# Kernel tuning notes

Hardware: AMD Instinct MI355X
Metric: run time of the kernel (lower is better)

Reference implementation:

```python
import jax, jax.numpy as jnp
import numpy as np

WIN, SHIFT = 8, 4
DIM, HEADS, MLP_H = 96, 6, 384
B, H, W = 1, 512, 512
HEAD_D = DIM // HEADS
N = WIN * WIN
EPS = 1e-5


def _rel_pos_index():
    ch = np.arange(WIN)
    coords = np.stack(np.meshgrid(ch, ch, indexing='ij')).reshape(2, -1)  # [2, 64]
    rel = (coords[:, :, None] - coords[:, None, :]).transpose(1, 2, 0)    # [64, 64, 2]
    rel[:, :, 0] += WIN - 1
    rel[:, :, 1] += WIN - 1
    rel[:, :, 0] *= 2 * WIN - 1
    return rel.sum(-1)


def _attn_mask():
    img = np.zeros((H, W))
    cnt = 0
    for hs in (slice(0, -WIN), slice(-WIN, -SHIFT), slice(-SHIFT, None)):
        for ws in (slice(0, -WIN), slice(-WIN, -SHIFT), slice(-SHIFT, None)):
            img[hs, ws] = cnt
            cnt += 1
    mw = img.reshape(H // WIN, WIN, W // WIN, WIN).transpose(0, 2, 1, 3).reshape(-1, N)
    diff = mw[:, None, :] - mw[:, :, None]
    return np.where(diff != 0, -100.0, 0.0).astype(np.float32)  # [nW, 64, 64]


REL_IDX = jnp.asarray(_rel_pos_index())
ATTN_MASK = jnp.asarray(_attn_mask())


def layernorm(x, w, b):
    mu = jnp.mean(x, axis=-1, keepdims=True)
    var = jnp.mean(jnp.square(x - mu), axis=-1, keepdims=True)
    return (x - mu) * jax.lax.rsqrt(var + EPS) * w + b


def setup_inputs() -> dict:
    key = jax.random.key(0)
    ks = jax.random.split(key, 16)
    s = 0.02
    return {
        'x': jax.random.normal(ks[0], (B, DIM, H, W), jnp.float32),
        'norm1_w': jnp.ones((DIM,), jnp.float32),
        'norm1_b': jnp.zeros((DIM,), jnp.float32),
        'qkv_w': jax.random.normal(ks[1], (3 * DIM, DIM), jnp.float32) * s,
        'qkv_b': jnp.zeros((3 * DIM,), jnp.float32),
        'rpb': jax.random.normal(ks[2], ((2 * WIN - 1) ** 2, HEADS), jnp.float32) * s,
        'proj_w': jax.random.normal(ks[3], (DIM, DIM), jnp.float32) * s,
        'proj_b': jnp.zeros((DIM,), jnp.float32),
        'norm2_w': jnp.ones((DIM,), jnp.float32),
        'norm2_b': jnp.zeros((DIM,), jnp.float32),
        'fc1_w': jax.random.normal(ks[4], (MLP_H, DIM), jnp.float32) * s,
        'fc1_b': jnp.zeros((MLP_H,), jnp.float32),
        'fc2_w': jax.random.normal(ks[5], (DIM, MLP_H), jnp.float32) * s,
        'fc2_b': jnp.zeros((DIM,), jnp.float32),
    }


def reference(x, norm1_w, norm1_b, qkv_w, qkv_b, rpb, proj_w, proj_b,
              norm2_w, norm2_b, fc1_w, fc1_b, fc2_w, fc2_b):
    nH, nW_ = H // WIN, W // WIN
    nWin = nH * nW_
    shortcut = jnp.transpose(x, (0, 2, 3, 1))            # [B,H,W,C]
    xn = layernorm(shortcut, norm1_w, norm1_b)
    xs = jnp.roll(xn, (-SHIFT, -SHIFT), axis=(1, 2))     # cyclic shift
    # window partition -> [B*nWin, N, C]
    win = xs.reshape(B, nH, WIN, nW_, WIN, DIM).transpose(0, 1, 3, 2, 4, 5)
    win = win.reshape(B * nWin, N, DIM)
    qkv = win @ qkv_w.T + qkv_b                          # [Bw, N, 3C]
    qkv = qkv.reshape(-1, N, 3, HEADS, HEAD_D).transpose(2, 0, 3, 1, 4)
    q, k, v = qkv[0], qkv[1], qkv[2]                     # [Bw, h, N, d]
    scale = HEAD_D ** -0.5
    attn = jnp.einsum('bhnd,bhmd->bhnm', q * scale, k)   # [Bw, h, 64, 64]
    bias = rpb[REL_IDX.reshape(-1)].reshape(N, N, HEADS).transpose(2, 0, 1)
    attn = attn + bias[None]
    attn = attn.reshape(B, nWin, HEADS, N, N) + ATTN_MASK[None, :, None]
    attn = jax.nn.softmax(attn.reshape(-1, HEADS, N, N), axis=-1)
    out = jnp.einsum('bhnm,bhmd->bhnd', attn, v).transpose(0, 2, 1, 3).reshape(-1, N, DIM)
    out = out @ proj_w.T + proj_b
    # window reverse + un-shift
    out = out.reshape(B, nH, nW_, WIN, WIN, DIM).transpose(0, 1, 3, 2, 4, 5).reshape(B, H, W, DIM)
    out = jnp.roll(out, (SHIFT, SHIFT), axis=(1, 2))
    x1 = shortcut + out
    h = layernorm(x1, norm2_w, norm2_b)
    h = jax.nn.gelu(h @ fc1_w.T + fc1_b, approximate=False) @ fc2_w.T + fc2_b
    x2 = x1 + h
    return jnp.transpose(x2, (0, 3, 1, 2))               # [B,C,H,W]
```

## Files before the change

kernel.cpp:

```cpp
#include <hip/hip_runtime.h>
#include <math.h>

#define WINSZ  8
#define SHIFTV 4
#define DIM    96
#define HEADS  6
#define HEAD_D 16
#define MLP_H  384
#define HH     512
#define WWID   512
#define HWSZ   (HH*WWID)
#define NTOK   64
#define EPSV   1e-5f
#define XP     97
#define QP     17
#define BFP    120

#define L2E    1.44269504088896f
#define QSC    0.360673760222f

#define OFF_W1   0
#define OFF_W2   36864
#define OFF_QKV  73728
#define OFF_PROJ 101376
#define OFF_BIAS 110592
#define WS_FULL  208896
#define WS_MLP   73728

#define QKP 104
#define VTP 72
#define X1P 97
#define WBP 104

#define WBA_OFF 13312
#define WBB_OFF 23296
#define SMEM_SZ 40448

typedef __attribute__((ext_vector_type(2))) short  s2v;
typedef __attribute__((ext_vector_type(4))) short  s4v;
typedef __attribute__((ext_vector_type(8))) short  s8v;
typedef __attribute__((ext_vector_type(4))) float  f4v;
typedef __attribute__((ext_vector_type(4))) unsigned short u4v;

__device__ __forceinline__ unsigned short f2bf(float v) {
    union { float f; unsigned u; } c; c.f = v;
    unsigned r = c.u + 0x7fffu + ((c.u >> 16) & 1u);
    return (unsigned short)(r >> 16);
}
__device__ __forceinline__ float bf2f(unsigned short u) {
    union { unsigned u; float f; } c; c.u = ((unsigned)u) << 16; return c.f;
}
__device__ __forceinline__ unsigned pk2(float a, float b) {
    unsigned r;
    asm("v_cvt_pk_bf16_f32 %0, %1, %2" : "=v"(r) : "v"(a), "v"(b));
    return r;
}
__device__ __forceinline__ s4v pk4(f4v v) {
    union { unsigned u[2]; s4v s; } o;
    o.u[0] = pk2(v[0], v[1]);
    o.u[1] = pk2(v[2], v[3]);
    return o.s;
}
__device__ __forceinline__ float fexp2(float x) {
#if __has_builtin(__builtin_amdgcn_exp2f)
    return __builtin_amdgcn_exp2f(x);
#else
    return exp2f(x);
#endif
}
__device__ __forceinline__ unsigned long long shfl64(unsigned long long v, int src) {
    union { unsigned long long q; int i[2]; } c; c.q = v;
    c.i[0] = __shfl(c.i[0], src);
    c.i[1] = __shfl(c.i[1], src);
    return c.q;
}
__device__ __forceinline__ float fast_gelu(float h) {
    float h2 = h*h;
    float u  = fmaf(0.044715f, h2, 1.0f);
    float e  = fexp2(-2.3022082f * h * u);
    return h * __builtin_amdgcn_rcpf(1.0f + e);
}

__device__ __forceinline__ void gld_lds16(const void* g, void* l) {
    __builtin_amdgcn_global_load_lds(
        (const __attribute__((address_space(1))) unsigned*)(g),
        (__attribute__((address_space(3))) unsigned*)(l),
        16, 0, 0);
}

__device__ __forceinline__ void stage48(const char* gb, int stride_b,
                                        char* wb, int tid) {
    #pragma unroll
    for (int k = 0; k < 3; ++k) {
        int idx = tid + k*256;
        if (k < 2 || idx < 624) {
            int r   = idx / 13;
            int rem = idx - r*13;
            const char* src = (rem < 12) ? (gb + r*stride_b + rem*16) : gb;
            char* dst = wb + ((tid & ~63) + k*256)*16;
            gld_lds16(src, dst);
        }
    }
}

__device__ __forceinline__ void stage_chunk(const char* w1B, const char* w2B,
                                            int n, char* dst, int tid) {
    int ch = n >> 2, s = n & 3;
    const char* src; int stride;
    if      (s == 0) { src = w1B + ch*96*192;            stride = 192; }
    else if (s == 1) { src = w1B + ch*96*192 + 48*192;   stride = 192; }
    else if (s == 2) { src = w2B + ch*192;               stride = 768; }
    else             { src = w2B + ch*192 + 48*768;      stride = 768; }
    stage48(src, stride, dst, tid);
}

__global__ __launch_bounds__(256) void conv_all(
    const float* __restrict__ qkvw, const float* __restrict__ projw,
    const float* __restrict__ f1w,  const float* __restrict__ f2w,
    const float* __restrict__ rpb,  short* __restrict__ ws)
{
    int i = (blockIdx.x*256 + threadIdx.x)*4;
    if (i < 110592) {
        const float* src; int off;
        if (i < 36864)       { src = f1w;  off = i;          }
        else if (i < 73728)  { src = f2w;  off = i - 36864;  }
        else if (i < 101376) { src = qkvw; off = i - 73728;  }
        else                 { src = projw; off = i - 101376; }
        f4v v = *(const f4v*)&src[off];
        s4v o;
        #pragma unroll
        for (int j = 0; j < 4; ++j) o[j] = (short)f2bf(v[j]);
        *(s4v*)&ws[i] = o;
    } else if (i < WS_FULL) {
        int idx = i - 110592;
        int tb = idx / 24576;
        int rm = idx - tb*24576;
        int hd = rm >> 12;
        int rc = rm & 4095;
        int r = rc >> 6, c0 = rc & 63;
        int rti = r>>3, rtj = r&7;
        int bh = tb>>1, bw = tb&1;
        int rhr = bh ? (rti<4?1:2) : 0;
        int rwr = bw ? (rtj<4?1:2) : 0;
        s4v o;
        #pragma unroll
        for (int j = 0; j < 4; ++j) {
            int c = c0 + j;
            int cti = c>>3, ctj = c&7;
            int rel = (rti-cti+7)*15 + (rtj-ctj+7);
            float b = rpb[rel*HEADS + hd];
            int rhc = bh ? (cti<4?1:2) : 0;
            int rwc = bw ? (ctj<4?1:2) : 0;
            if (rhr != rhc || rwr != rwc) b -= 100.f;
            o[j] = (short)f2bf(b * L2E);
        }
        *(s4v*)&ws[OFF_BIAS + idx] = o;
    }
}

__global__ __launch_bounds__(256,4) void fused_kernel(
    const float* __restrict__ x,
    const float* __restrict__ n1w, const float* __restrict__ n1b,
    const float* __restrict__ qkvb, const float* __restrict__ projb,
    const float* __restrict__ n2w, const float* __restrict__ n2b,
    const float* __restrict__ f1b, const float* __restrict__ f2b,
    const short* __restrict__ wqkv, const short* __restrict__ wproj,
    const short* __restrict__ w1b, const short* __restrict__ w2b,
    const short* __restrict__ btab,
    float* __restrict__ out)
{
    __shared__ __align__(16) char smem[SMEM_SZ];
    short* qb   = (short*)smem;
    short* kb2  = (short*)(smem + 13312);
    short* vT   = (short*)(smem + 26624);
    short* aob  = qb;
    short* lnb2 = (short*)smem;
    short* hid  = (short*)smem;
    short* wbA  = (short*)(smem + WBA_OFF);
    short* wbB  = (short*)(smem + WBB_OFF);
    float* x1f  = (float*)smem;

    const int tid  = threadIdx.x;
    const int wv   = tid >> 6, lane = tid & 63;
    const int col  = lane & 15, kq = lane >> 4;
    const int trow = wv*16 + col;

    int bid = blockIdx.x;
    int wl = (bid & 7)*512 + ((bid >> 5) << 2) + ((bid >> 3) & 3);
    const int wi = wl >> 6, wj = wl & 63;

    const int ti = trow>>3, tj = trow&7;
    const int hpos = (wi*8 + ti + SHIFTV) & (HH-1);
    const int wpos = (wj*8 + tj + SHIFTV) & (WWID-1);
    const int p = hpos*WWID + wpos;

    s8v bfr[3];
    {
        float v[24], s1 = 0.f, s2 = 0.f;
        #pragma unroll
        for (int kb = 0; kb < 3; ++kb)
            #pragma unroll
            for (int j = 0; j < 8; ++j) {
                float vv = x[(kb*32 + kq*8 + j)*HWSZ + p];
                v[kb*8+j] = vv; s1 += vv; s2 += vv*vv;
            }
        s1 += __shfl_xor(s1, 16); s2 += __shfl_xor(s2, 16);
        s1 += __shfl_xor(s1, 32); s2 += __shfl_xor(s2, 32);
        float mu = s1*(1.f/96.f);
        float rs = rsqrtf(s2*(1.f/96.f) - mu*mu + EPSV);
        #pragma unroll
        for (int kb = 0; kb < 3; ++kb) {
            f4v wA = *(const f4v*)&n1w[kb*32 + kq*8];
            f4v wB = *(const f4v*)&n1w[kb*32 + kq*8 + 4];
            f4v bA = *(const f4v*)&n1b[kb*32 + kq*8];
            f4v bB = *(const f4v*)&n1b[kb*32 + kq*8 + 4];
            float a[8];
            #pragma unroll
            for (int j = 0; j < 4; ++j) {
                a[j]   = (v[kb*8+j]  -mu)*rs*wA[j] + bA[j];
                a[4+j] = (v[kb*8+4+j]-mu)*rs*wB[j] + bB[j];
            }
            union { unsigned u[4]; s8v s; } o;
            #pragma unroll
            for (int j = 0; j < 4; ++j) o.u[j] = pk2(a[2*j], a[2*j+1]);
            bfr[kb] = o.s;
        }
    }

    float shc[24];
    #pragma unroll
    for (int mt = 0; mt < 6; ++mt)
        #pragma unroll
        for (int i = 0; i < 4; ++i)
            shc[mt*4+i] = x[(mt*16 + kq*4 + i)*HWSZ + p];

    const s8v zfrag = {0,0,0,0,0,0,0,0};

    {
        #pragma unroll
        for (int g = 0; g < 6; ++g) {
            s8v aw[9];
            #pragma unroll
            for (int m = 0; m < 3; ++m)
                #pragma unroll
                for (int kb = 0; kb < 3; ++kb)
                    aw[m*3+kb] = *(const s8v*)&wqkv[((g*3+m)*16+col)*96 + kb*32 + kq*8];
            #pragma unroll
            for (int m = 0; m < 3; ++m) {
                int mt = g*3 + m;
                f4v acc = {0.f,0.f,0.f,0.f};
                #pragma unroll
                for (int kb = 0; kb < 3; ++kb)
                    acc = __builtin_amdgcn_mfma_f32_16x16x32_bf16(aw[m*3+kb], bfr[kb], acc, 0,0,0);
                int od0 = mt*16 + kq*4;
                f4v bia = *(const f4v*)&qkvb[od0];
                if (mt < 6) {
                    f4v t;
                    #pragma unroll
                    for (int i = 0; i < 4; ++i) t[i] = (acc[i]+bia[i])*QSC;
                    *(s4v*)&qb[trow*QKP + od0] = pk4(t);
                } else if (mt < 12) {
                    f4v t;
                    #pragma unroll
                    for (int i = 0; i < 4; ++i) t[i] = acc[i]+bia[i];
                    *(s4v*)&kb2[trow*QKP + od0 - 96] = pk4(t);
                } else {
                    int d0 = od0 - 192;
                    f4v t;
                    #pragma unroll
                    for (int i = 0; i < 4; ++i) t[i] = acc[i]+bia[i];
                    s4v o = pk4(t);
                    #pragma unroll
                    for (int i = 0; i < 4; ++i)
                        vT[(d0+i)*VTP + trow] = o[i];
                }
            }
        }
    }
    __syncthreads();

    const int tb = ((wi==63)?2:0) | ((wj==63)?1:0);
    u4v bt[4];
    {
        const short* gb = btab + ((tb*6+0)<<12) + (trow<<6);
        #pragma unroll
        for (int mt = 0; mt < 4; ++mt) bt[mt] = *(const u4v*)&gb[mt*16 + kq*4];
    }
    for (int hd = 0; hd < 6; ++hd) {
        u4v btn[4];
        if (hd < 5) {
            const short* gb = btab + ((tb*6+hd+1)<<12) + (trow<<6);
            #pragma unroll
            for (int mt = 0; mt < 4; ++mt) btn[mt] = *(const u4v*)&gb[mt*16 + kq*4];
        }
        s8v bq = zfrag;
        if (kq < 2) bq = *(const s8v*)&qb[trow*QKP + hd*16 + kq*8];
        f4v st[4];
        #pragma unroll
        for (int mt = 0; mt < 4; ++mt) {
            s8v a = zfrag;
            if (kq < 2) a = *(const s8v*)&kb2[(mt*16+col)*QKP + hd*16 + kq*8];
            f4v z = {0.f,0.f,0.f,0.f};
            st[mt] = __builtin_amdgcn_mfma_f32_16x16x32_bf16(a, bq, z, 0,0,0);
        }
        float pe[16];
        #pragma unroll
        for (int mt = 0; mt < 4; ++mt)
            #pragma unroll
            for (int i = 0; i < 4; ++i)
                pe[mt*4+i] = fexp2(st[mt][i] + bf2f(bt[mt][i]));
        float s8r[8];
        #pragma unroll
        for (int j = 0; j < 8; ++j) s8r[j] = pe[2*j] + pe[2*j+1];
        #pragma unroll
        for (int j = 0; j < 4; ++j) s8r[j] += s8r[j+4];
        float sum = (s8r[0]+s8r[2]) + (s8r[1]+s8r[3]);
        sum += __shfl_xor(sum, 16);
        sum += __shfl_xor(sum, 32);
        unsigned long long p64[4];
        #pragma unroll
        for (int mt = 0; mt < 4; ++mt) {
            union { unsigned u[2]; unsigned long long q; } pq;
            pq.u[0] = pk2(pe[mt*4+0], pe[mt*4+1]);
            pq.u[1] = pk2(pe[mt*4+2], pe[mt*4+3]);
            p64[mt] = pq.q;
        }
        const int s0 = col + ((kq & 1) << 5);
        const int sel = kq >> 1;
        f4v g = {0.f,0.f,0.f,0.f};
        #pragma unroll
        for (int c = 0; c < 2; ++c) {
            unsigned long long t0 = shfl64(p64[2*c],   s0);
            unsigned long long t1 = shfl64(p64[2*c+1], s0);
            unsigned long long lo = sel ? t1 : t0;
            unsigned long long u0 = shfl64(p64[2*c],   s0+16);
            unsigned long long u1 = shfl64(p64[2*c+1], s0+16);
            unsigned long long hi = sel ? u1 : u0;
            union { unsigned long long q[2]; s8v v; } bb;
            bb.q[0] = lo; bb.q[1] = hi;
            s8v a = *(const s8v*)&vT[(hd*16+col)*VTP + c*32 + kq*8];
            g = __builtin_amdgcn_mfma_f32_16x16x32_bf16(a, bb.v, g, 0,0,0);
        }
        float linv = __builtin_amdgcn_rcpf(sum);
        f4v gl;
        #pragma unroll
        for (int i = 0; i < 4; ++i) gl[i] = g[i]*linv;
        *(s4v*)&aob[trow*QKP + hd*16 + kq*4] = pk4(gl);
        #pragma unroll
        for (int mt = 0; mt < 4; ++mt) bt[mt] = btn[mt];
    }
    __syncthreads();

    stage_chunk((const char*)w1b, (const char*)w2b, 0, (char*)wbA, tid);
    stage_chunk((const char*)w1b, (const char*)w2b, 1, (char*)wbB, tid);

    float x1r[24];
    {
        s8v bfr2[3];
        #pragma unroll
        for (int kb = 0; kb < 3; ++kb)
            bfr2[kb] = *(const s8v*)&aob[trow*QKP + kb*32 + kq*8];
        #pragma unroll
        for (int g = 0; g < 2; ++g) {
            s8v aw[9];
            #pragma unroll
            for (int m = 0; m < 3; ++m)
                #pragma unroll
                for (int kb = 0; kb < 3; ++kb)
                    aw[m*3+kb] = *(const s8v*)&wproj[((g*3+m)*16+col)*96 + kb*32 + kq*8];
            #pragma unroll
            for (int m = 0; m < 3; ++m) {
                int mt = g*3 + m;
                f4v acc = {0.f,0.f,0.f,0.f};
                #pragma unroll
                for (int kb = 0; kb < 3; ++kb)
                    acc = __builtin_amdgcn_mfma_f32_16x16x32_bf16(aw[m*3+kb], bfr2[kb], acc, 0,0,0);
                int c0 = mt*16 + kq*4;
                f4v pb4 = *(const f4v*)&projb[c0];
                #pragma unroll
                for (int i = 0; i < 4; ++i)
                    x1r[mt*4+i] = shc[mt*4+i] + acc[i] + pb4[i];
            }
        }
    }

    const int mrow = wv*16;

    {
        float s1 = 0.f, s2 = 0.f;
        #pragma unroll
        for (int j = 0; j < 24; ++j) { s1 += x1r[j]; s2 += x1r[j]*x1r[j]; }
        s1 += __shfl_xor(s1, 16); s2 += __shfl_xor(s2, 16);
        s1 += __shfl_xor(s1, 32); s2 += __shfl_xor(s2, 32);
        float mu = s1*(1.f/96.f);
        float rs = rsqrtf(s2*(1.f/96.f) - mu*mu + EPSV);
        #pragma unroll
        for (int mt = 0; mt < 6; ++mt) {
            int c0 = mt*16 + kq*4;
            f4v w4 = *(const f4v*)&n2w[c0];
            f4v b4 = *(const f4v*)&n2b[c0];
            f4v t;
            #pragma unroll
            for (int i = 0; i < 4; ++i)
                t[i] = (x1r[mt*4+i]-mu)*rs*w4[i] + b4[i];
            *(s4v*)&lnb2[trow*QKP + c0] = pk4(t);
        }
    }
    __threadfence_block();

    s8v a1[3];
    #pragma unroll
    for (int kb = 0; kb < 3; ++kb)
        a1[kb] = *(const s8v*)&lnb2[(mrow+col)*QKP + kb*32 + kq*8];

    f4v acc2[6];
    #pragma unroll
    for (int n = 0; n < 6; ++n) acc2[n] = (f4v){0.f,0.f,0.f,0.f};

    __syncthreads();

    #pragma unroll
    for (int ch = 0; ch < 4; ++ch) {
        #pragma unroll
        for (int sub = 0; sub < 2; ++sub) {
            const int cidx = ch*4 + sub;
            const short* wb = (cidx & 1) ? wbB : wbA;
            #pragma unroll
            for (int nl = 0; nl < 3; ++nl) {
                f4v acc = (f4v){0.f,0.f,0.f,0.f};
                #pragma unroll
                for (int kb = 0; kb < 3; ++kb) {
                    s8v b = *(const s8v*)&wb[(nl*16+col)*WBP + kb*32 + kq*8];
                    acc = __builtin_amdgcn_mfma_f32_16x16x32_bf16(a1[kb], b, acc, 0,0,0);
                }
                int cch = sub*48 + nl*16 + col;
                float bias = f1b[ch*96 + cch];
                f4v t;
                #pragma unroll
                for (int i = 0; i < 4; ++i) t[i] = fast_gelu(acc[i]+bias);
                s4v o = pk4(t);
                #pragma unroll
                for (int i = 0; i < 4; ++i)
                    hid[(mrow + kq*4 + i)*QKP + cch] = o[i];
            }
            __syncthreads();
            if (cidx + 2 < 16)
                stage_chunk((const char*)w1b, (const char*)w2b, cidx+2,
                            (char*)((cidx & 1) ? wbB : wbA), tid);
        }
        s8v a2[3];
        #pragma unroll
        for (int kb = 0; kb < 3; ++kb)
            a2[kb] = *(const s8v*)&hid[(mrow+col)*QKP + kb*32 + kq*8];
        #pragma unroll
        for (int sub = 0; sub < 2; ++sub) {
            const int cidx = ch*4 + 2 + sub;
            const short* wb = (cidx & 1) ? wbB : wbA;
            #pragma unroll
            for (int nl = 0; nl < 3; ++nl) {
                int nt = sub*3 + nl;
                #pragma unroll
                for (int kb = 0; kb < 3; ++kb) {
                    s8v b = *(const s8v*)&wb[(nl*16+col)*WBP + kb*32 + kq*8];
                    acc2[nt] = __builtin_amdgcn_mfma_f32_16x16x32_bf16(a2[kb], b, acc2[nt], 0,0,0);
                }
            }
            __syncthreads();
            if (cidx + 2 < 16)
                stage_chunk((const char*)w1b, (const char*)w2b, cidx+2,
                            (char*)((cidx & 1) ? wbB : wbA), tid);
        }
    }

    #pragma unroll
    for (int mt = 0; mt < 6; ++mt) {
        #pragma unroll
        for (int i = 0; i < 4; ++i)
            x1f[trow*X1P + mt*16 + kq*4 + i] = x1r[mt*4+i];
    }
    __threadfence_block();
    #pragma unroll
    for (int nt = 0; nt < 6; ++nt) {
        int c = nt*16 + col;
        float bias = f2b[c];
        #pragma unroll
        for (int i = 0; i < 4; ++i) {
            int t = mrow + kq*4 + i;
            x1f[t*X1P + c] += acc2[nt][i] + bias;
        }
    }
    __threadfence_block();
    {
        int tt = mrow + col;
        int tti = tt>>3, ttj = tt&7;
        int pp = ((wi*8 + tti + SHIFTV) & (HH-1))*WWID + ((wj*8 + ttj + SHIFTV) & (WWID-1));
        #pragma unroll
        for (int it = 0; it < 24; ++it) {
            int c = it*4 + kq;
            out[c*HWSZ + pp] = x1f[tt*X1P + c];
        }
    }
}

__global__ __launch_bounds__(256) void attn_kernel(
    const float* __restrict__ x,
    const float* __restrict__ n1w, const float* __restrict__ n1b,
    const float* __restrict__ qkvw, const float* __restrict__ qkvb,
    const float* __restrict__ rpb,
    const float* __restrict__ projw, const float* __restrict__ projb,
    float* __restrict__ out)
{
    __shared__ float xn[NTOK*XP];
    __shared__ float ao[NTOK*XP];
    __shared__ float qh[NTOK*QP];
    __shared__ float kh[NTOK*QP];
    __shared__ float vh[NTOK*QP];
    __shared__ int   srid[NTOK];
    __shared__ int   spos[NTOK];

    const int tid = threadIdx.x;
    const int blk = blockIdx.x;
    const int wi = blk >> 6, wj = blk & 63;

    {
        int t  = tid >> 2;
        int j4 = tid & 3;
        int ti = t >> 3, tj = t & 7;
        int a = wi*WINSZ + ti;
        int bcol = wj*WINSZ + tj;
        int h = (a + SHIFTV) & (HH-1);
        int w = (bcol + SHIFTV) & (WWID-1);
        int p = h*WWID + w;
        if (j4 == 0) {
            spos[t] = p;
            int rh = (a < HH-WINSZ) ? 0 : (a < HH-SHIFTV ? 1 : 2);
            int rw = (bcol < WWID-WINSZ) ? 0 : (bcol < WWID-SHIFTV ? 1 : 2);
            srid[t] = rh*3 + rw;
        }
        float xv[24];
        float s1 = 0.f, s2 = 0.f;
        int c0 = j4*24;
        #pragma unroll
        for (int i = 0; i < 24; ++i) {
            float v = x[(c0+i)*HWSZ + p];
            xv[i] = v; s1 += v; s2 += v*v;
        }
        s1 += __shfl_xor(s1,1); s2 += __shfl_xor(s2,1);
        s1 += __shfl_xor(s1,2); s2 += __shfl_xor(s2,2);
        float mu  = s1 * (1.f/96.f);
        float var = s2 * (1.f/96.f) - mu*mu;
        float rs  = rsqrtf(var + EPSV);
        #pragma unroll
        for (int i = 0; i < 24; ++i) {
            int c = c0 + i;
            xn[t*XP + c] = (xv[i]-mu)*rs*n1w[c] + n1b[c];
        }
    }
    __syncthreads();

    const int wv   = tid >> 6;
    const int lane = tid & 63;
    const int r    = tid >> 2;
    const int g    = tid & 3;
    const int rti  = r >> 3, rtj = r & 7;

    for (int hd = 0; hd < HEADS; ++hd) {
        for (int it = 0; it < 12; ++it) {
            int ol = it*4 + wv;
            int s = ol >> 4, d = ol & 15;
            int grow = __builtin_amdgcn_readfirstlane(s*DIM + hd*HEAD_D + d);
            const float* wr = qkvw + grow*DIM;
            float acc = qkvb[grow];
            #pragma unroll 8
            for (int c = 0; c < DIM; ++c)
                acc = fmaf(xn[lane*XP+c], wr[c], acc);
            float* dst = (s==0) ? qh : ((s==1) ? kh : vh);
            dst[lane*QP + d] = acc;
        }
        __syncthreads();

        float qr[16];
        #pragma unroll
        for (int d = 0; d < 16; ++d) qr[d] = qh[r*QP+d];
        float scr[16];
        int myrid = srid[r];
        #pragma unroll
        for (int jj = 0; jj < 16; ++jj) {
            int colx = g*16 + jj;
            float a = 0.f;
            #pragma unroll
            for (int d = 0; d < 16; ++d) a = fmaf(qr[d], kh[colx*QP+d], a);
            int cti = colx >> 3, ctj = colx & 7;
            int rel = (rti - cti + 7)*15 + (rtj - ctj + 7);
            float b = rpb[rel*HEADS + hd];
            float m = (srid[colx]==myrid) ? 0.f : -100.f;
            scr[jj] = a*0.25f + b + m;
        }
        float mx = scr[0];
        #pragma unroll
        for (int jj = 1; jj < 16; ++jj) mx = fmaxf(mx, scr[jj]);
        mx = fmaxf(mx, __shfl_xor(mx,1));
        mx = fmaxf(mx, __shfl_xor(mx,2));
        float sum = 0.f;
        #pragma unroll
        for (int jj = 0; jj < 16; ++jj) { scr[jj] = __expf(scr[jj]-mx); sum += scr[jj]; }
        sum += __shfl_xor(sum,1);
        sum += __shfl_xor(sum,2);
        float inv = 1.f/sum;
        #pragma unroll
        for (int d = 0; d < 16; ++d) {
            float a = 0.f;
            #pragma unroll
            for (int jj = 0; jj < 16; ++jj) a = fmaf(scr[jj], vh[(g*16+jj)*QP+d], a);
            a += __shfl_xor(a,1);
            a += __shfl_xor(a,2);
            if (g == 0) ao[r*XP + hd*HEAD_D + d] = a*inv;
        }
        __syncthreads();
    }

    for (int it = 0; it < 24; ++it) {
        int c = __builtin_amdgcn_readfirstlane(it*4 + wv);
        const float* wr = projw + c*DIM;
        float acc = projb[c];
        #pragma unroll 8
        for (int k = 0; k < DIM; ++k)
            acc = fmaf(ao[lane*XP+k], wr[k], acc);
        int p2 = spos[lane];
        float shc = x[c*HWSZ + p2];
        out[c*HWSZ + p2] = shc + acc;
    }
}

__global__ __launch_bounds__(256) void mlp_mfma(
    float* __restrict__ io,
    const float* __restrict__ n2w, const float* __restrict__ n2b,
    const short* __restrict__ w1b, const float* __restrict__ f1b,
    const short* __restrict__ w2b, const float* __restrict__ f2b)
{
    __shared__ short lnbuf[64*BFP];
    __shared__ __align__(16) char ubuf[64*XP*4];
    float* lnf = (float*)ubuf;
    short* hbc = (short*)ubuf;

    const int tid  = threadIdx.x;
    const int base = blockIdx.x * 64;

    for (int idx = tid; idx < 64*DIM; idx += 256) {
        int c = idx >> 6, t = idx & 63;
        lnf[t*XP + c] = io[c*HWSZ + base + t];
    }
    __syncthreads();
    {
        int t = tid >> 2, q = tid & 3;
        float xv[24], s1 = 0.f, s2 = 0.f;
        #pragma unroll
        for (int i = 0; i < 24; ++i) {
            float v = lnf[t*XP + q*24 + i]; xv[i] = v; s1 += v; s2 += v*v;
        }
        s1 += __shfl_xor(s1,1); s2 += __shfl_xor(s2,1);
        s1 += __shfl_xor(s1,2); s2 += __shfl_xor(s2,2);
        float mu = s1*(1.f/96.f);
        float rs = rsqrtf(s2*(1.f/96.f) - mu*mu + EPSV);
        #pragma unroll
        for (int i = 0; i < 24; ++i) {
            int c = q*24 + i;
            lnbuf[t*BFP + c] = (short)f2bf((xv[i]-mu)*rs*n2w[c] + n2b[c]);
        }
    }
    __syncthreads();

    const int l = tid & 63, wv = tid >> 6;
    const int mrow = wv*16;
    const int col = l & 15, kq = l >> 4;

    s8v a1[3];
    #pragma unroll
    for (int kb = 0; kb < 3; ++kb)
        a1[kb] = *(const s8v*)&lnbuf[(mrow+col)*BFP + kb*32 + kq*8];

    f4v acc2[6];
    #pragma unroll
    for (int n = 0; n < 6; ++n) acc2[n] = (f4v){0.f,0.f,0.f,0.f};

    for (int ch = 0; ch < 4; ++ch) {
        #pragma unroll
        for (int nt = 0; nt < 6; ++nt) {
            int n0 = ch*96 + nt*16;
            f4v acc = (f4v){0.f,0.f,0.f,0.f};
            #pragma unroll
            for (int kb = 0; kb < 3; ++kb) {
                s8v b = *(const s8v*)&w1b[(n0+col)*96 + kb*32 + kq*8];
                acc = __builtin_amdgcn_mfma_f32_16x16x32_bf16(a1[kb], b, acc, 0, 0, 0);
            }
            float bias = f1b[n0+col];
            #pragma unroll
            for (int i = 0; i < 4; ++i) {
                float g = fast_gelu(acc[i] + bias);
                hbc[(mrow + kq*4 + i)*BFP + nt*16 + col] = (short)f2bf(g);
            }
        }
        __threadfence_block();
        s8v a2[3];
        #pragma unroll
        for (int kb = 0; kb < 3; ++kb)
            a2[kb] = *(const s8v*)&hbc[(mrow+col)*BFP + kb*32 + kq*8];
        #pragma unroll
        for (int nt = 0; nt < 6; ++nt) {
            #pragma unroll
            for (int kb = 0; kb < 3; ++kb) {
                s8v b = *(const s8v*)&w2b[(nt*16+col)*MLP_H + ch*96 + kb*32 + kq*8];
                acc2[nt] = __builtin_amdgcn_mfma_f32_16x16x32_bf16(a2[kb], b, acc2[nt], 0, 0, 0);
            }
        }
        __threadfence_block();
    }

    #pragma unroll
    for (int nt = 0; nt < 6; ++nt) {
        int c = nt*16 + col;
        float bias = f2b[c];
        #pragma unroll
        for (int i = 0; i < 4; ++i) {
            int t = mrow + kq*4 + i;
            float* p = &io[c*HWSZ + base + t];
            *p = *p + acc2[nt][i] + bias;
        }
    }
}

__global__ __launch_bounds__(256) void conv_w(
    const float* __restrict__ f1w, const float* __restrict__ f2w,
    short* __restrict__ ws)
{
    int i = blockIdx.x*256 + threadIdx.x;
    if (i < 36864)      ws[i] = (short)f2bf(f1w[i]);
    else if (i < 73728) ws[i] = (short)f2bf(f2w[i-36864]);
}

extern "C" void kernel_launch(void* const* d_in, const int* in_sizes, int n_in,
                              void* d_out, int out_size, void* d_ws, size_t ws_size,
                              hipStream_t stream) {
    const float* x     = (const float*)d_in[0];
    const float* n1w   = (const float*)d_in[1];
    const float* n1b   = (const float*)d_in[2];
    const float* qkvw  = (const float*)d_in[3];
    const float* qkvb  = (const float*)d_in[4];
    const float* rpb   = (const float*)d_in[5];
    const float* projw = (const float*)d_in[6];
    const float* projb = (const float*)d_in[7];
    const float* n2w   = (const float*)d_in[8];
    const float* n2b   = (const float*)d_in[9];
    const float* f1w   = (const float*)d_in[10];
    const float* f1b   = (const float*)d_in[11];
    const float* f2w   = (const float*)d_in[12];
    const float* f2b   = (const float*)d_in[13];
    float* out = (float*)d_out;

    if (ws_size >= (size_t)WS_FULL * sizeof(short)) {
        short* wsb = (short*)d_ws;
        hipLaunchKernelGGL(conv_all, dim3(204), dim3(256), 0, stream,
                           qkvw, projw, f1w, f2w, rpb, wsb);
        hipLaunchKernelGGL(fused_kernel, dim3(4096), dim3(256), 0, stream,
                           x, n1w, n1b, qkvb, projb, n2w, n2b, f1b, f2b,
                           wsb + OFF_QKV, wsb + OFF_PROJ,
                           wsb + OFF_W1, wsb + OFF_W2, wsb + OFF_BIAS, out);
    } else {
        short* wsb = (short*)d_ws;
        hipLaunchKernelGGL(attn_kernel, dim3(4096), dim3(256), 0, stream,
                           x, n1w, n1b, qkvw, qkvb, rpb, projw, projb, out);
        hipLaunchKernelGGL(conv_w, dim3(288), dim3(256), 0, stream, f1w, f2w, wsb);
        hipLaunchKernelGGL(mlp_mfma, dim3(4096), dim3(256), 0, stream,
                           out, n2w, n2b, wsb, f1b, wsb + 36864, f2b);
    }
}
```

Measured before the change: 391.9 us.

## Load MLP weights directly to registers with double-buffered prefetch instead of LDS staging

```diff
diff --git a/kernel.cpp b/kernel.cpp
--- a/kernel.cpp
+++ b/kernel.cpp
@@ -29,11 +29,8 @@
 
 #define QKP 104
 #define VTP 72
-#define X1P 97
-#define WBP 104
-
-#define WBA_OFF 13312
-#define WBB_OFF 23296
+#define X1P 100
+
 #define SMEM_SZ 40448
 
 typedef __attribute__((ext_vector_type(2))) short  s2v;
@@ -79,39 +76,6 @@
     float u  = fmaf(0.044715f, h2, 1.0f);
     float e  = fexp2(-2.3022082f * h * u);
     return h * __builtin_amdgcn_rcpf(1.0f + e);
-}
-
-__device__ __forceinline__ void gld_lds16(const void* g, void* l) {
-    __builtin_amdgcn_global_load_lds(
-        (const __attribute__((address_space(1))) unsigned*)(g),
-        (__attribute__((address_space(3))) unsigned*)(l),
-        16, 0, 0);
-}
-
-__device__ __forceinline__ void stage48(const char* gb, int stride_b,
-                                        char* wb, int tid) {
-    #pragma unroll
-    for (int k = 0; k < 3; ++k) {
-        int idx = tid + k*256;
-        if (k < 2 || idx < 624) {
-            int r   = idx / 13;
-            int rem = idx - r*13;
-            const char* src = (rem < 12) ? (gb + r*stride_b + rem*16) : gb;
-            char* dst = wb + ((tid & ~63) + k*256)*16;
-            gld_lds16(src, dst);
-        }
-    }
-}
-
-__device__ __forceinline__ void stage_chunk(const char* w1B, const char* w2B,
-                                            int n, char* dst, int tid) {
-    int ch = n >> 2, s = n & 3;
-    const char* src; int stride;
-    if      (s == 0) { src = w1B + ch*96*192;            stride = 192; }
-    else if (s == 1) { src = w1B + ch*96*192 + 48*192;   stride = 192; }
-    else if (s == 2) { src = w2B + ch*192;               stride = 768; }
-    else             { src = w2B + ch*192 + 48*768;      stride = 768; }
-    stage48(src, stride, dst, tid);
 }
 
 __global__ __launch_bounds__(256) void conv_all(
@@ -174,16 +138,15 @@
     short* kb2  = (short*)(smem + 13312);
     short* vT   = (short*)(smem + 26624);
     short* aob  = qb;
-    short* lnb2 = (short*)smem;
-    short* hid  = (short*)smem;
-    short* wbA  = (short*)(smem + WBA_OFF);
-    short* wbB  = (short*)(smem + WBB_OFF);
-    float* x1f  = (float*)smem;
+    short* lnb2 = qb;
+    short* hid  = qb;
+    float* x1p  = (float*)(smem + 13312);
 
     const int tid  = threadIdx.x;
     const int wv   = tid >> 6, lane = tid & 63;
     const int col  = lane & 15, kq = lane >> 4;
     const int trow = wv*16 + col;
+    const int mrow = wv*16;
 
     int bid = blockIdx.x;
     int wl = (bid & 7)*512 + ((bid >> 5) << 2) + ((bid >> 3) & 3);
@@ -237,21 +200,21 @@
     const s8v zfrag = {0,0,0,0,0,0,0,0};
 
     {
-        #pragma unroll
-        for (int g = 0; g < 6; ++g) {
-            s8v aw[9];
+        auto qkv_pre = [&](int g, s8v (&w)[9]) {
             #pragma unroll
             for (int m = 0; m < 3; ++m)
                 #pragma unroll
                 for (int kb = 0; kb < 3; ++kb)
-                    aw[m*3+kb] = *(const s8v*)&wqkv[((g*3+m)*16+col)*96 + kb*32 + kq*8];
+                    w[m*3+kb] = *(const s8v*)&wqkv[((g*3+m)*16+col)*96 + kb*32 + kq*8];
+        };
+        auto qkv_cmp = [&](int g, const s8v (&w)[9]) {
             #pragma unroll
             for (int m = 0; m < 3; ++m) {
                 int mt = g*3 + m;
                 f4v acc = {0.f,0.f,0.f,0.f};
                 #pragma unroll
                 for (int kb = 0; kb < 3; ++kb)
-                    acc = __builtin_amdgcn_mfma_f32_16x16x32_bf16(aw[m*3+kb], bfr[kb], acc, 0,0,0);
+                    acc = __builtin_amdgcn_mfma_f32_16x16x32_bf16(w[m*3+kb], bfr[kb], acc, 0,0,0);
                 int od0 = mt*16 + kq*4;
                 f4v bia = *(const f4v*)&qkvb[od0];
                 if (mt < 6) {
@@ -275,6 +238,15 @@
                         vT[(d0+i)*VTP + trow] = o[i];
                 }
             }
+        };
+        s8v qwA[9], qwB[9];
+        qkv_pre(0, qwA);
+        #pragma unroll
+        for (int gp = 0; gp < 3; ++gp) {
+            qkv_pre(2*gp+1, qwB);
+            qkv_cmp(2*gp,   qwA);
+            if (gp < 2) qkv_pre(2*gp+2, qwA);
+            qkv_cmp(2*gp+1, qwB);
         }
     }
     __syncthreads();
@@ -351,40 +323,31 @@
     }
     __syncthreads();
 
-    stage_chunk((const char*)w1b, (const char*)w2b, 0, (char*)wbA, tid);
-    stage_chunk((const char*)w1b, (const char*)w2b, 1, (char*)wbB, tid);
-
     float x1r[24];
     {
         s8v bfr2[3];
         #pragma unroll
         for (int kb = 0; kb < 3; ++kb)
             bfr2[kb] = *(const s8v*)&aob[trow*QKP + kb*32 + kq*8];
-        #pragma unroll
-        for (int g = 0; g < 2; ++g) {
-            s8v aw[9];
-            #pragma unroll
-            for (int m = 0; m < 3; ++m)
-                #pragma unroll
-                for (int kb = 0; kb < 3; ++kb)
-                    aw[m*3+kb] = *(const s8v*)&wproj[((g*3+m)*16+col)*96 + kb*32 + kq*8];
-            #pragma unroll
-            for (int m = 0; m < 3; ++m) {
-                int mt = g*3 + m;
-                f4v acc = {0.f,0.f,0.f,0.f};
-                #pragma unroll
-                for (int kb = 0; kb < 3; ++kb)
-                    acc = __builtin_amdgcn_mfma_f32_16x16x32_bf16(aw[m*3+kb], bfr2[kb], acc, 0,0,0);
-                int c0 = mt*16 + kq*4;
-                f4v pb4 = *(const f4v*)&projb[c0];
-                #pragma unroll
-                for (int i = 0; i < 4; ++i)
-                    x1r[mt*4+i] = shc[mt*4+i] + acc[i] + pb4[i];
-            }
-        }
-    }
-
-    const int mrow = wv*16;
+        s8v pw[18];
+        #pragma unroll
+        for (int mt = 0; mt < 6; ++mt)
+            #pragma unroll
+            for (int kb = 0; kb < 3; ++kb)
+                pw[mt*3+kb] = *(const s8v*)&wproj[(mt*16+col)*96 + kb*32 + kq*8];
+        #pragma unroll
+        for (int mt = 0; mt < 6; ++mt) {
+            f4v acc = {0.f,0.f,0.f,0.f};
+            #pragma unroll
+            for (int kb = 0; kb < 3; ++kb)
+                acc = __builtin_amdgcn_mfma_f32_16x16x32_bf16(pw[mt*3+kb], bfr2[kb], acc, 0,0,0);
+            int c0 = mt*16 + kq*4;
+            f4v pb4 = *(const f4v*)&projb[c0];
+            #pragma unroll
+            for (int i = 0; i < 4; ++i)
+                x1r[mt*4+i] = shc[mt*4+i] + acc[i] + pb4[i];
+        }
+    }
 
     {
         float s1 = 0.f, s2 = 0.f;
@@ -408,32 +371,46 @@
     }
     __threadfence_block();
 
-    s8v a1[3];
+    #pragma unroll
+    for (int mt = 0; mt < 6; ++mt) {
+        f4v t;
+        #pragma unroll
+        for (int i = 0; i < 4; ++i) t[i] = x1r[mt*4+i];
+        *(f4v*)&x1p[trow*X1P + mt*16 + kq*4] = t;
+    }
+
+    s8v a1[3], a2[3];
     #pragma unroll
     for (int kb = 0; kb < 3; ++kb)
         a1[kb] = *(const s8v*)&lnb2[(mrow+col)*QKP + kb*32 + kq*8];
+    __threadfence_block();
 
     f4v acc2[6];
     #pragma unroll
     for (int n = 0; n < 6; ++n) acc2[n] = (f4v){0.f,0.f,0.f,0.f};
 
-    __syncthreads();
-
-    #pragma unroll
-    for (int ch = 0; ch < 4; ++ch) {
-        #pragma unroll
-        for (int sub = 0; sub < 2; ++sub) {
-            const int cidx = ch*4 + sub;
-            const short* wb = (cidx & 1) ? wbB : wbA;
+    auto mlp_pre = [&](int ph, s8v (&w)[9]) {
+        const int ch = ph >> 2, q = ph & 3;
+        #pragma unroll
+        for (int nl = 0; nl < 3; ++nl)
+            #pragma unroll
+            for (int kb = 0; kb < 3; ++kb) {
+                if (q < 2)
+                    w[nl*3+kb] = *(const s8v*)&w1b[(ch*96 + q*48 + nl*16 + col)*96 + kb*32 + kq*8];
+                else
+                    w[nl*3+kb] = *(const s8v*)&w2b[((q-2)*48 + nl*16 + col)*MLP_H + ch*96 + kb*32 + kq*8];
+            }
+    };
+    auto mlp_phase = [&](int ph, const s8v (&w)[9]) {
+        const int ch = ph >> 2, q = ph & 3;
+        if (q < 2) {
             #pragma unroll
             for (int nl = 0; nl < 3; ++nl) {
                 f4v acc = (f4v){0.f,0.f,0.f,0.f};
                 #pragma unroll
-                for (int kb = 0; kb < 3; ++kb) {
-                    s8v b = *(const s8v*)&wb[(nl*16+col)*WBP + kb*32 + kq*8];
-                    acc = __builtin_amdgcn_mfma_f32_16x16x32_bf16(a1[kb], b, acc, 0,0,0);
-                }
-                int cch = sub*48 + nl*16 + col;
+                for (int kb = 0; kb < 3; ++kb)
+                    acc = __builtin_amdgcn_mfma_f32_16x16x32_bf16(a1[kb], w[nl*3+kb], acc, 0,0,0);
+                int cch = q*48 + nl*16 + col;
                 float bias = f1b[ch*96 + cch];
                 f4v t;
                 #pragma unroll
@@ -443,41 +420,35 @@
                 for (int i = 0; i < 4; ++i)
                     hid[(mrow + kq*4 + i)*QKP + cch] = o[i];
             }
-            __syncthreads();
-            if (cidx + 2 < 16)
-                stage_chunk((const char*)w1b, (const char*)w2b, cidx+2,
-                            (char*)((cidx & 1) ? wbB : wbA), tid);
-        }
-        s8v a2[3];
-        #pragma unroll
-        for (int kb = 0; kb < 3; ++kb)
-            a2[kb] = *(const s8v*)&hid[(mrow+col)*QKP + kb*32 + kq*8];
-        #pragma unroll
-        for (int sub = 0; sub < 2; ++sub) {
-            const int cidx = ch*4 + 2 + sub;
-            const short* wb = (cidx & 1) ? wbB : wbA;
+            if (q == 1) {
+                __threadfence_block();
+                #pragma unroll
+                for (int kb = 0; kb < 3; ++kb)
+                    a2[kb] = *(const s8v*)&hid[(mrow+col)*QKP + kb*32 + kq*8];
+            }
+        } else {
             #pragma unroll
             for (int nl = 0; nl < 3; ++nl) {
-                int nt = sub*3 + nl;
+                int nt = (q-2)*3 + nl;
                 #pragma unroll
-                for (int kb = 0; kb < 3; ++kb) {
-                    s8v b = *(const s8v*)&wb[(nl*16+col)*WBP + kb*32 + kq*8];
-                    acc2[nt] = __builtin_amdgcn_mfma_f32_16x16x32_bf16(a2[kb], b, acc2[nt], 0,0,0);
-                }
-            }
-            __syncthreads();
-            if (cidx + 2 < 16)
-                stage_chunk((const char*)w1b, (const char*)w2b, cidx+2,
-                            (char*)((cidx & 1) ? wbB : wbA), tid);
-        }
-    }
-
-    #pragma unroll
-    for (int mt = 0; mt < 6; ++mt) {
-        #pragma unroll
-        for (int i = 0; i < 4; ++i)
-            x1f[trow*X1P + mt*16 + kq*4 + i] = x1r[mt*4+i];
-    }
+                for (int kb = 0; kb < 3; ++kb)
+                    acc2[nt] = __builtin_amdgcn_mfma_f32_16x16x32_bf16(a2[kb], w[nl*3+kb], acc2[nt], 0,0,0);
+            }
+        }
+    };
+
+    {
+        s8v wA[9], wB[9];
+        mlp_pre(0, wA);
+        #pragma unroll
+        for (int pp = 0; pp < 8; ++pp) {
+            mlp_pre(2*pp+1, wB);
+            mlp_phase(2*pp, wA);
+            if (pp < 7) mlp_pre(2*pp+2, wA);
+            mlp_phase(2*pp+1, wB);
+        }
+    }
+
     __threadfence_block();
     #pragma unroll
     for (int nt = 0; nt < 6; ++nt) {
@@ -486,7 +457,7 @@
         #pragma unroll
         for (int i = 0; i < 4; ++i) {
             int t = mrow + kq*4 + i;
-            x1f[t*X1P + c] += acc2[nt][i] + bias;
+            x1p[t*X1P + c] += acc2[nt][i] + bias;
         }
     }
     __threadfence_block();
@@ -497,7 +468,7 @@
         #pragma unroll
         for (int it = 0; it < 24; ++it) {
             int c = it*4 + kq;
-            out[c*HWSZ + pp] = x1f[tt*X1P + c];
+            out[c*HWSZ + pp] = x1p[tt*X1P + c];
         }
     }
 }
```

Result: slower. 544.6 us (+39.0%).

## Stage full 96-row MLP weight chunks, halving barriers in the MLP loop

Applied to the files above, without the earlier changes.

```diff
diff --git a/kernel.cpp b/kernel.cpp
--- a/kernel.cpp
+++ b/kernel.cpp
@@ -33,8 +33,8 @@
 #define WBP 104
 
 #define WBA_OFF 13312
-#define WBB_OFF 23296
-#define SMEM_SZ 40448
+#define WBB_OFF 33280
+#define SMEM_SZ 53248
 
 typedef __attribute__((ext_vector_type(2))) short  s2v;
 typedef __attribute__((ext_vector_type(4))) short  s4v;
@@ -88,12 +88,12 @@
         16, 0, 0);
 }
 
-__device__ __forceinline__ void stage48(const char* gb, int stride_b,
+__device__ __forceinline__ void stage96(const char* gb, int stride_b,
                                         char* wb, int tid) {
     #pragma unroll
-    for (int k = 0; k < 3; ++k) {
+    for (int k = 0; k < 5; ++k) {
         int idx = tid + k*256;
-        if (k < 2 || idx < 624) {
+        if (k < 4 || idx < 1248) {
             int r   = idx / 13;
             int rem = idx - r*13;
             const char* src = (rem < 12) ? (gb + r*stride_b + rem*16) : gb;
@@ -103,15 +103,11 @@
     }
 }
 
-__device__ __forceinline__ void stage_chunk(const char* w1B, const char* w2B,
-                                            int n, char* dst, int tid) {
-    int ch = n >> 2, s = n & 3;
-    const char* src; int stride;
-    if      (s == 0) { src = w1B + ch*96*192;            stride = 192; }
-    else if (s == 1) { src = w1B + ch*96*192 + 48*192;   stride = 192; }
-    else if (s == 2) { src = w2B + ch*192;               stride = 768; }
-    else             { src = w2B + ch*192 + 48*768;      stride = 768; }
-    stage48(src, stride, dst, tid);
+__device__ __forceinline__ void stage_chunk8(const char* w1B, const char* w2B,
+                                             int n, char* dst, int tid) {
+    int ch = n >> 1;
+    if (n & 1) stage96(w2B + ch*192, 768, dst, tid);
+    else       stage96(w1B + ch*96*192, 192, dst, tid);
 }
 
 __global__ __launch_bounds__(256) void conv_all(
@@ -158,7 +154,7 @@
     }
 }
 
-__global__ __launch_bounds__(256,4) void fused_kernel(
+__global__ __launch_bounds__(256,3) void fused_kernel(
     const float* __restrict__ x,
     const float* __restrict__ n1w, const float* __restrict__ n1b,
     const float* __restrict__ qkvb, const float* __restrict__ projb,
@@ -174,16 +170,17 @@
     short* kb2  = (short*)(smem + 13312);
     short* vT   = (short*)(smem + 26624);
     short* aob  = qb;
-    short* lnb2 = (short*)smem;
-    short* hid  = (short*)smem;
+    short* lnb2 = qb;
+    short* hid  = qb;
     short* wbA  = (short*)(smem + WBA_OFF);
     short* wbB  = (short*)(smem + WBB_OFF);
-    float* x1f  = (float*)smem;
+    float* x1f  = (float*)(smem + WBA_OFF);
 
     const int tid  = threadIdx.x;
     const int wv   = tid >> 6, lane = tid & 63;
     const int col  = lane & 15, kq = lane >> 4;
     const int trow = wv*16 + col;
+    const int mrow = wv*16;
 
     int bid = blockIdx.x;
     int wl = (bid & 7)*512 + ((bid >> 5) << 2) + ((bid >> 3) & 3);
@@ -351,8 +348,8 @@
     }
     __syncthreads();
 
-    stage_chunk((const char*)w1b, (const char*)w2b, 0, (char*)wbA, tid);
-    stage_chunk((const char*)w1b, (const char*)w2b, 1, (char*)wbB, tid);
+    stage_chunk8((const char*)w1b, (const char*)w2b, 0, (char*)wbA, tid);
+    stage_chunk8((const char*)w1b, (const char*)w2b, 1, (char*)wbB, tid);
 
     float x1r[24];
     {
@@ -383,8 +380,6 @@
             }
         }
     }
-
-    const int mrow = wv*16;
 
     {
         float s1 = 0.f, s2 = 0.f;
@@ -408,7 +403,7 @@
     }
     __threadfence_block();
 
-    s8v a1[3];
+    s8v a1[3], a2[3];
     #pragma unroll
     for (int kb = 0; kb < 3; ++kb)
         a1[kb] = *(const s8v*)&lnb2[(mrow+col)*QKP + kb*32 + kq*8];
@@ -420,20 +415,19 @@
     __syncthreads();
 
     #pragma unroll
-    for (int ch = 0; ch < 4; ++ch) {
-        #pragma unroll
-        for (int sub = 0; sub < 2; ++sub) {
-            const int cidx = ch*4 + sub;
-            const short* wb = (cidx & 1) ? wbB : wbA;
-            #pragma unroll
-            for (int nl = 0; nl < 3; ++nl) {
+    for (int ph = 0; ph < 8; ++ph) {
+        const short* wb = (ph & 1) ? wbB : wbA;
+        const int ch = ph >> 1;
+        if ((ph & 1) == 0) {
+            #pragma unroll
+            for (int nl = 0; nl < 6; ++nl) {
                 f4v acc = (f4v){0.f,0.f,0.f,0.f};
                 #pragma unroll
                 for (int kb = 0; kb < 3; ++kb) {
                     s8v b = *(const s8v*)&wb[(nl*16+col)*WBP + kb*32 + kq*8];
                     acc = __builtin_amdgcn_mfma_f32_16x16x32_bf16(a1[kb], b, acc, 0,0,0);
                 }
-                int cch = sub*48 + nl*16 + col;
+                int cch = nl*16 + col;
                 float bias = f1b[ch*96 + cch];
                 f4v t;
                 #pragma unroll
@@ -443,33 +437,24 @@
                 for (int i = 0; i < 4; ++i)
                     hid[(mrow + kq*4 + i)*QKP + cch] = o[i];
             }
-            __syncthreads();
-            if (cidx + 2 < 16)
-                stage_chunk((const char*)w1b, (const char*)w2b, cidx+2,
-                            (char*)((cidx & 1) ? wbB : wbA), tid);
-        }
-        s8v a2[3];
-        #pragma unroll
-        for (int kb = 0; kb < 3; ++kb)
-            a2[kb] = *(const s8v*)&hid[(mrow+col)*QKP + kb*32 + kq*8];
-        #pragma unroll
-        for (int sub = 0; sub < 2; ++sub) {
-            const int cidx = ch*4 + 2 + sub;
-            const short* wb = (cidx & 1) ? wbB : wbA;
-            #pragma unroll
-            for (int nl = 0; nl < 3; ++nl) {
-                int nt = sub*3 + nl;
+            __threadfence_block();
+            #pragma unroll
+            for (int kb = 0; kb < 3; ++kb)
+                a2[kb] = *(const s8v*)&hid[(mrow+col)*QKP + kb*32 + kq*8];
+        } else {
+            #pragma unroll
+            for (int nl = 0; nl < 6; ++nl) {
                 #pragma unroll
                 for (int kb = 0; kb < 3; ++kb) {
                     s8v b = *(const s8v*)&wb[(nl*16+col)*WBP + kb*32 + kq*8];
-                    acc2[nt] = __builtin_amdgcn_mfma_f32_16x16x32_bf16(a2[kb], b, acc2[nt], 0,0,0);
+                    acc2[nl] = __builtin_amdgcn_mfma_f32_16x16x32_bf16(a2[kb], b, acc2[nl], 0,0,0);
                 }
             }
-            __syncthreads();
-            if (cidx + 2 < 16)
-                stage_chunk((const char*)w1b, (const char*)w2b, cidx+2,
-                            (char*)((cidx & 1) ? wbB : wbA), tid);
-        }
+        }
+        __syncthreads();
+        if (ph + 2 < 8)
+            stage_chunk8((const char*)w1b, (const char*)w2b, ph+2,
+                         (char*)((ph & 1) ? wbB : wbA), tid);
     }
 
     #pragma unroll
```

Measured after the change: 373.4 us. -4.7%, faster.
